# Optimization experiments

Hardware: AMD Instinct MI355X
Metric: run time of the kernel (lower is better)

The kernel has to match this reference:

```python
import jax, jax.numpy as jnp
import numpy as np

B, L, T = 512, 1024, 128  # batch, seq_len, n_tags


def setup_inputs() -> dict:
    key = jax.random.key(0)
    k1, k2, k3 = jax.random.split(key, 3)
    return {
        "emit_scores": jax.random.normal(k1, (B, L, T), dtype=jnp.float32),
        "transitions": jax.random.normal(k2, (T, T), dtype=jnp.float32),
        "tag_weight": jax.random.uniform(k3, (T,), dtype=jnp.float32),
    }


def _viterbi_single(emit, transitions):
    # emit: [L, T] (already scaled by tag_weight); transitions: [T, T]
    def step(prev, obs):
        # scores[i, j] = prev[i] + obs[j] + transitions[i, j]
        scores = prev[:, None] + obs[None, :] + transitions  # [T, T]
        return jnp.max(scores, axis=0), jnp.argmax(scores, axis=0).astype(jnp.int32)

    prev, bps = jax.lax.scan(step, emit[0], emit[1:])  # bps: [L-1, T]
    best_score = jnp.max(prev)
    last = jnp.argmax(prev).astype(jnp.int32)

    # Backtrace: path[t] = bps[t][path[t+1]], path[L-1] = last
    def back(idx, bp):
        nidx = bp[idx]
        return nidx, nidx

    _, rev_path = jax.lax.scan(back, last, bps, reverse=True)  # [L-1]
    path = jnp.concatenate([rev_path, last[None]])  # [L]
    return path, best_score


def reference(emit_scores, transitions, tag_weight):
    # emit_scores *= tag_weight (broadcast over tag dim), matching the torch code
    emit = emit_scores * tag_weight  # [B, L, T]
    path, best_score = jax.vmap(_viterbi_single, in_axes=(0, None))(emit, transitions)
    # path: [B, L] int32 tag indices (the original maps these to tag strings);
    # best_score: [B] Viterbi max score.
    return path, best_score
```

## Files before the change

kernel.cpp:

```cpp
#include <hip/hip_runtime.h>

#define B 512
#define L 1024
#define T 128
#define NROWS (L - 1)
#define SEG 64
#define NSEG 16

typedef unsigned char u8;
typedef float f2 __attribute__((ext_vector_type(2)));

#define M3(a, b, c) fmaxf(fmaxf((a), (b)), (c))

static __device__ __forceinline__ f2 pkadd(f2 a, f2 b) {
    f2 d;
    asm("v_pk_add_f32 %0, %1, %2" : "=v"(d) : "v"(a), "v"(b));
    return d;
}
static __device__ __forceinline__ float mx3(float a, float b, float c) {
    float d;
    asm("v_max3_f32 %0, %1, %2, %3" : "=v"(d) : "v"(a), "v"(b), "v"(c));
    return d;
}

#define DPPMAX(v, CTRL)                                                        \
    fmaxf((v), __int_as_float(__builtin_amdgcn_mov_dpp(                        \
                   __float_as_int(v), (CTRL), 0xf, 0xf, true)))
#define SWZMAX(v)                                                              \
    fmaxf((v), __int_as_float(__builtin_amdgcn_ds_swizzle(                     \
                   __float_as_int(v), 0x101F)))

#define BAR()                                                  \
    do {                                                       \
        asm volatile("s_waitcnt lgkmcnt(0)" ::: "memory");     \
        __builtin_amdgcn_s_barrier();                          \
        asm volatile("" ::: "memory");                         \
    } while (0)


__global__ __launch_bounds__(1024, 8) void viterbi_fwd_val(
    const float* __restrict__ emit, const float* __restrict__ trans,
    const float* __restrict__ w, float* __restrict__ out,
    float* __restrict__ prevws, int* __restrict__ lastTag)
{
    const int b   = blockIdx.x;
    const int tid = threadIdx.x;
    const int h   = tid & 7;
    const int j   = tid >> 3;
    const int hbase = h << 4;

    __shared__ __align__(16) float prevbuf[2 * T];
    __shared__ float swv[16];
    __shared__ int   swj[16];

    f2 tc2[8];
#pragma unroll
    for (int q = 0; q < 4; ++q) {
        f2 a, c;
        a.x = trans[(size_t)(hbase + 4 * q + 0) * T + j];
        a.y = trans[(size_t)(hbase + 4 * q + 1) * T + j];
        c.x = trans[(size_t)(hbase + 4 * q + 2) * T + j];
        c.y = trans[(size_t)(hbase + 4 * q + 3) * T + j];
        tc2[2 * q] = a; tc2[2 * q + 1] = c;
    }

    const float wj = w[j];
    const size_t ebase = (size_t)b * L * T;
    float* prow = prevws + (size_t)b * NROWS * T;

    const int ro0 = 16 * ((4 * h + 0) ^ ((h >> 1) & 3));
    const int ro1 = 16 * ((4 * h + 1) ^ ((h >> 1) & 3));
    const int ro2 = 16 * ((4 * h + 2) ^ ((h >> 1) & 3));
    const int ro3 = 16 * ((4 * h + 3) ^ ((h >> 1) & 3));
    const char* prdb = (const char*)prevbuf;
    char* pwr = (char*)prevbuf + 16 * ((j >> 2) ^ ((j >> 5) & 3)) + 4 * (j & 3);

    const float e0 = emit[ebase + j] * wj;
    if (h == 0) *(float*)pwr = e0;
    if (h == 1) prow[j] = e0;
    float myprev = e0;
    float r_c = emit[ebase + (size_t)T + j];
    float r_1 = emit[ebase + (size_t)2 * T + j];
    float bv_prev = 0.0f;
    BAR();

#define STEP(T_, ROFF_, WOFF_)                                                 \
    {                                                                          \
        const int t_ = (T_);                                                   \
        if (h == 1 && t_ >= 2)                        \
            prow[(size_t)(t_ - 1) * T + j] = bv_prev;                          \
        const int tn_ = (t_ + 2 < L) ? (t_ + 2) : (L - 1);                     \
        const float r_2 = emit[ebase + (size_t)tn_ * T + j];                   \
        const float obs_ = r_c * wj;                                           \
        f2 od_; od_.x = obs_; od_.y = obs_;                                    \
        const float4 p0 = *(const float4*)(prdb + (ROFF_) + ro0);              \
        const float4 p1 = *(const float4*)(prdb + (ROFF_) + ro1);              \
        const float4 p2 = *(const float4*)(prdb + (ROFF_) + ro2);              \
        const float4 p3 = *(const float4*)(prdb + (ROFF_) + ro3);              \
        f2 q0; q0.x = p0.x; q0.y = p0.y;                                       \
        f2 q1; q1.x = p0.z; q1.y = p0.w;                                       \
        f2 q2; q2.x = p1.x; q2.y = p1.y;                                       \
        f2 q3; q3.x = p1.z; q3.y = p1.w;                                       \
        f2 q4; q4.x = p2.x; q4.y = p2.y;                                       \
        f2 q5; q5.x = p2.z; q5.y = p2.w;                                       \
        f2 q6; q6.x = p3.x; q6.y = p3.y;                                       \
        f2 q7; q7.x = p3.z; q7.y = p3.w;                                       \
        const f2 v0 = pkadd(pkadd(q0, od_), tc2[0]);                           \
        const f2 v1 = pkadd(pkadd(q1, od_), tc2[1]);                           \
        const f2 v2 = pkadd(pkadd(q2, od_), tc2[2]);                           \
        const f2 v3 = pkadd(pkadd(q3, od_), tc2[3]);                           \
        const f2 v4 = pkadd(pkadd(q4, od_), tc2[4]);                           \
        const f2 v5 = pkadd(pkadd(q5, od_), tc2[5]);                           \
        const f2 v6 = pkadd(pkadd(q6, od_), tc2[6]);                           \
        const f2 v7 = pkadd(pkadd(q7, od_), tc2[7]);                           \
        const float m0 = mx3(v0.x, v0.y, v1.x);                               \
        const float m1 = mx3(v1.y, v2.x, v2.y);                               \
        const float m2 = mx3(v3.x, v3.y, v4.x);                               \
        const float m3 = mx3(v4.y, v5.x, v5.y);                               \
        const float m4 = mx3(v6.x, v6.y, v7.x);                               \
        const float n0 = mx3(m0, m1, m2);                                      \
        const float n1 = fmaxf(m3, m4);                                        \
        float bv = mx3(n0, n1, v7.y);                                          \
        bv = DPPMAX(bv, 0xB1);                          \
        bv = DPPMAX(bv, 0x4E);                          \
        bv = SWZMAX(bv);                               \
        if (h == 0) *(float*)(pwr + (WOFF_)) = bv;                             \
        myprev = bv;                                                           \
        bv_prev = bv;                                                          \
        r_c = r_1; r_1 = r_2;                                                  \
        BAR();                                                                 \
    }

    int t = 1;
    while (t + 1 < L) {
        STEP(t, 0, 512)
        STEP(t + 1, 512, 0)
        t += 2;
    }
    STEP(1023, 0, 512)
#undef STEP

    float rv = myprev; int rj = j;
#pragma unroll
    for (int m = 8; m <= 32; m <<= 1) {
        const float pv = __shfl_xor(rv, m);
        const int   pj = __shfl_xor(rj, m);
        if (pv > rv || (pv == rv && pj < rj)) { rv = pv; rj = pj; }
    }
    if ((tid & 63) == 0) { swv[tid >> 6] = rv; swj[tid >> 6] = rj; }
    __syncthreads();
    if (tid == 0) {
        float fv = swv[0]; int fj = swj[0];
#pragma unroll
        for (int wv = 1; wv < 16; ++wv) {
            if (swv[wv] > fv || (swv[wv] == fv && swj[wv] < fj)) {
                fv = swv[wv]; fj = swj[wv];
            }
        }
        out[(size_t)B * L + b] = fv;
        out[(size_t)b * L + (L - 1)] = (float)fj;
        lastTag[b] = fj;
    }
}

__global__ __launch_bounds__(64, 1) void backtrace(
    const float* __restrict__ emit, const float* __restrict__ trans,
    const float* __restrict__ w, const float* __restrict__ prevws,
    const int* __restrict__ lastTag, float* __restrict__ out)
{
    const int b = blockIdx.x;
    const int lane = threadIdx.x;
    __shared__ float transT[T * T];

#pragma unroll 4
    for (int it = 0; it < (T * T) / 64; ++it) {
        const int k = it * 64 + lane;
        const int i = k >> 7, jj = k & 127;
        transT[jj * T + (i ^ (jj & 31))] = trans[k];
    }

    const float w0 = w[lane], w1 = w[lane + 64];
    const size_t pbase = (size_t)b * NROWS * T;
    const size_t ebase = (size_t)b * L * T;
    const size_t obase = (size_t)b * L;

    float rp0[8], rp1[8], re0[8], re1[8];
#pragma unroll
    for (int k = 0; k < 8; ++k) {
        rp0[k] = prevws[pbase + (size_t)(1022 - k) * T + lane];
        rp1[k] = prevws[pbase + (size_t)(1022 - k) * T + lane + 64];
        re0[k] = emit[ebase + (size_t)(1023 - k) * T + lane];
        re1[k] = emit[ebase + (size_t)(1023 - k) * T + lane + 64];
    }

    int idx = lastTag[b];
    const float bsc = out[(size_t)B * L + b];
    float pp0 = bsc, pp1 = bsc;
    __syncthreads();

    int r = 1022;

#define BODY(U_)                                                               \
    {                                                                          \
        const float c0_ = rp0[U_], c1_ = rp1[U_];                              \
        const float e0_ = re0[U_], e1_ = re1[U_];                              \
        const int pr = (r >= 8) ? (r - 8) : 0;                                 \
        rp0[U_] = prevws[pbase + (size_t)pr * T + lane];                       \
        rp1[U_] = prevws[pbase + (size_t)pr * T + lane + 64];                  \
        re0[U_] = emit[ebase + (size_t)(pr + 1) * T + lane];                   \
        re1[U_] = emit[ebase + (size_t)(pr + 1) * T + lane + 64];              \
        const int sl = idx & 63;                                               \
        const bool lo = idx < 64;                                              \
        const float bv  = __shfl(lo ? pp0 : pp1, sl);                          \
        const float ew0 = e0_ * w0, ew1 = e1_ * w1;                            \
        const float obs = __shfl(lo ? ew0 : ew1, sl);                          \
        const int xc = lane ^ (idx & 31);                                      \
        const float t0 = transT[idx * T + xc];                                 \
        const float t1 = transT[idx * T + 64 + xc];                            \
        const float s0 = (c0_ + obs) + t0;                                     \
        const float s1 = (c1_ + obs) + t1;                                     \
        const unsigned long long m0 = __ballot(s0 == bv);                      \
        const unsigned long long m1 = __ballot(s1 == bv);                      \
        idx = (m0 != 0ULL) ? __builtin_ctzll(m0)                               \
                           : 64 + __builtin_ctzll(m1);                         \
        if (lane == 0) out[obase + r] = (float)idx;                            \
        pp0 = c0_; pp1 = c1_;                                                  \
        --r;                                                                   \
    }

#pragma unroll 1
    for (int g = 0; g < 127; ++g) {
        BODY(0) BODY(1) BODY(2) BODY(3) BODY(4) BODY(5) BODY(6) BODY(7)
    }
    BODY(0) BODY(1) BODY(2) BODY(3) BODY(4) BODY(5) BODY(6)
#undef BODY
}

__global__ __launch_bounds__(512, 4) void viterbi_fwd_slow(
    const float* __restrict__ emit, const float* __restrict__ trans,
    const float* __restrict__ w, float* __restrict__ out,
    u8* __restrict__ bps, int* __restrict__ lastTag)
{
    const int b   = blockIdx.x;
    const int tid = threadIdx.x;
    const int h   = tid & 3;
    const int j   = tid >> 2;
    const int hbase = h << 5;
    const bool lane0 = (h == 0);
    const int INF = 0x7fffffff;

    __shared__ __align__(16) float prevbuf[2 * T];
    __shared__ float swv[8];
    __shared__ int   swj[8];

    f2 tc2[16];
#pragma unroll
    for (int q = 0; q < 8; ++q) {
        f2 a, c;
        a.x = trans[(size_t)(hbase + 4 * q + 0) * T + j];
        a.y = trans[(size_t)(hbase + 4 * q + 1) * T + j];
        c.x = trans[(size_t)(hbase + 4 * q + 2) * T + j];
        c.y = trans[(size_t)(hbase + 4 * q + 3) * T + j];
        tc2[2 * q] = a; tc2[2 * q + 1] = c;
    }

    const float wj = w[j];
    const size_t ebase = (size_t)b * L * T;
    u8* bprow = bps + (size_t)b * NROWS * T;

    const char* prd = (const char*)prevbuf + 128 * h;
    char* pwr = (char*)prevbuf + 16 * ((j >> 2) ^ (j >> 5)) + 4 * (j & 3);

    const float e0 = emit[ebase + j] * wj;
    if (lane0) *(float*)pwr = e0;
    float myprev = e0;
    float raw_cur = emit[ebase + (size_t)T + j];
    int bidx_prev = 0;
    __syncthreads();

#define STEP(T_, ROFF_, WOFF_)                                                 \
    {                                                                          \
        const int t_ = (T_);                                                   \
        if (lane0 && t_ >= 2)                                                  \
            bprow[(size_t)(t_ - 2) * T + j] = (u8)bidx_prev;                   \
        const int tn_ = (t_ + 1 < L) ? (t_ + 1) : (L - 1);                     \
        const float raw_next_ = emit[ebase + (size_t)tn_ * T + j];             \
        const float obs_ = raw_cur * wj;                                       \
        f2 od_; od_.x = obs_; od_.y = obs_;                                    \
        f2 sv[16];                                                             \
        _Pragma("unroll")                                                      \
        for (int q = 0; q < 8; ++q) {                                          \
            const float4 p = *(const float4*)(prd + (ROFF_) + 16 * (q ^ h));   \
            f2 plo; plo.x = p.x; plo.y = p.y;                                  \
            f2 phi; phi.x = p.z; phi.y = p.w;                                  \
            sv[2 * q]     = (plo + od_) + tc2[2 * q];                          \
            sv[2 * q + 1] = (phi + od_) + tc2[2 * q + 1];                      \
        }                                                                      \
        float cm[4]; int loc[4];                                               \
        _Pragma("unroll")                                                      \
        for (int c = 0; c < 4; ++c) {                                          \
            const float s0 = sv[4 * c + 0].x, s1 = sv[4 * c + 0].y;            \
            const float s2 = sv[4 * c + 1].x, s3 = sv[4 * c + 1].y;            \
            const float s4 = sv[4 * c + 2].x, s5 = sv[4 * c + 2].y;            \
            const float s6 = sv[4 * c + 3].x, s7 = sv[4 * c + 3].y;            \
            const float m = M3(M3(s0, s1, s2), M3(s3, s4, s5),                 \
                               fmaxf(s6, s7));                                 \
            int k = 0;                                                         \
            k = (s7 == m) ? 7 : k; k = (s6 == m) ? 6 : k;                      \
            k = (s5 == m) ? 5 : k; k = (s4 == m) ? 4 : k;                      \
            k = (s3 == m) ? 3 : k; k = (s2 == m) ? 2 : k;                      \
            k = (s1 == m) ? 1 : k;                                             \
            cm[c] = m; loc[c] = 8 * c + k;                                     \
        }                                                                      \
        float bv = fmaxf(fmaxf(cm[0], cm[1]), fmaxf(cm[2], cm[3]));            \
        const int l0 = (cm[0] == bv) ? loc[0] : INF;                           \
        const int l1 = (cm[1] == bv) ? loc[1] : INF;                           \
        const int l2 = (cm[2] == bv) ? loc[2] : INF;                           \
        const int l3 = (cm[3] == bv) ? loc[3] : INF;                           \
        const int lm = min(min(min(l0, l1), l2), l3);                          \
        int gi = hbase + lm;                                                   \
        const float lv = bv;                                                   \
        bv = fmaxf(bv, __shfl_xor(bv, 1));                                     \
        bv = fmaxf(bv, __shfl_xor(bv, 2));                                     \
        int ii = (lv == bv) ? gi : INF;                                        \
        ii = min(ii, __shfl_xor(ii, 1));                                       \
        ii = min(ii, __shfl_xor(ii, 2));                                       \
        if (lane0) *(float*)(pwr + (WOFF_)) = bv;                              \
        myprev = bv;                                                           \
        bidx_prev = ii;                                                        \
        raw_cur = raw_next_;                                                   \
        __syncthreads();                                                       \
    }

    int t = 1;
    while (t + 1 < L) {
        STEP(t, 0, 512)
        STEP(t + 1, 512, 0)
        t += 2;
    }
    STEP(1023, 0, 512)
#undef STEP

    if (lane0) bprow[(size_t)(NROWS - 1) * T + j] = (u8)bidx_prev;

    float rv = myprev; int rj = j;
#pragma unroll
    for (int m = 4; m <= 32; m <<= 1) {
        const float pv = __shfl_xor(rv, m);
        const int   pj = __shfl_xor(rj, m);
        if (pv > rv || (pv == rv && pj < rj)) { rv = pv; rj = pj; }
    }
    if ((tid & 63) == 0) { swv[tid >> 6] = rv; swj[tid >> 6] = rj; }
    __syncthreads();
    if (tid == 0) {
        float fv = swv[0]; int fj = swj[0];
#pragma unroll
        for (int wv = 1; wv < 8; ++wv) {
            if (swv[wv] > fv || (swv[wv] == fv && swj[wv] < fj)) {
                fv = swv[wv]; fj = swj[wv];
            }
        }
        out[(size_t)B * L + b] = fv;
        out[(size_t)b * L + (L - 1)] = (float)fj;
        lastTag[b] = fj;
    }
}

__global__ __launch_bounds__(T) void segcomp(const u8* __restrict__ bps,
                                             u8* __restrict__ comp)
{
    const int s = blockIdx.x & (NSEG - 1);
    const int b = blockIdx.x >> 4;
    const int r0 = s * SEG;
    const int cnt = (NROWS - r0 < SEG) ? (NROWS - r0) : SEG;

    __shared__ __align__(16) u8 rows[SEG * T];
    const uint4* src = (const uint4*)(bps + ((size_t)b * NROWS + r0) * T);
    uint4* dst = (uint4*)rows;
    const int nvec = cnt * (T / 16);
    for (int k = threadIdx.x; k < nvec; k += T) dst[k] = src[k];
    __syncthreads();

    int x = threadIdx.x;
    for (int k = cnt - 1; k >= 0; --k) x = rows[k * T + x];
    comp[((size_t)b * NSEG + s) * T + threadIdx.x] = (u8)x;
}

__global__ void chainseg(const u8* __restrict__ comp,
                         const int* __restrict__ lastTag,
                         float* __restrict__ out)
{
    const int b = blockIdx.x * blockDim.x + threadIdx.x;
    if (b >= B) return;
    int e = lastTag[b];
#pragma unroll 1
    for (int s = NSEG - 1; s >= 0; --s) {
        e = comp[((size_t)b * NSEG + s) * T + e];
        out[(size_t)b * L + s * SEG] = (float)e;
    }
}

__global__ __launch_bounds__(T) void fillseg(const u8* __restrict__ bps,
                                             const int* __restrict__ lastTag,
                                             float* __restrict__ out)
{
    const int s = blockIdx.x & (NSEG - 1);
    const int b = blockIdx.x >> 4;
    const int r0 = s * SEG;
    const int cnt = (NROWS - r0 < SEG) ? (NROWS - r0) : SEG;

    __shared__ __align__(16) u8 rows[SEG * T];
    const uint4* src = (const uint4*)(bps + ((size_t)b * NROWS + r0) * T);
    uint4* dst = (uint4*)rows;
    const int nvec = cnt * (T / 16);
    for (int k = threadIdx.x; k < nvec; k += T) dst[k] = src[k];
    __syncthreads();

    if (threadIdx.x == 0) {
        int e = (s == NSEG - 1) ? lastTag[b]
                                : (int)out[(size_t)b * L + (size_t)(s + 1) * SEG];
        for (int k = cnt - 1; k >= 1; --k) {
            e = rows[k * T + e];
            out[(size_t)b * L + r0 + k] = (float)e;
        }
    }
}

extern "C" void kernel_launch(void* const* d_in, const int* in_sizes, int n_in,
                              void* d_out, int out_size, void* d_ws, size_t ws_size,
                              hipStream_t stream)
{
    const float* emit  = (const float*)d_in[0];
    const float* trans = (const float*)d_in[1];
    const float* w     = (const float*)d_in[2];
    float* out = (float*)d_out;

    const size_t prev_bytes = (size_t)B * NROWS * T * sizeof(float);
    const size_t need_fast  = prev_bytes + B * sizeof(int);

    if (ws_size >= need_fast) {
        float* prevws  = (float*)d_ws;
        int*   lastTag = (int*)((char*)d_ws + prev_bytes);
        viterbi_fwd_val<<<B, 1024, 0, stream>>>(emit, trans, w, out, prevws, lastTag);
        backtrace<<<B, 64, 0, stream>>>(emit, trans, w, prevws, lastTag, out);
    } else {
        u8*  bps     = (u8*)d_ws;
        u8*  comp    = bps + (size_t)B * NROWS * T;
        int* lastTag = (int*)(comp + (size_t)B * NSEG * T);
        viterbi_fwd_slow<<<B, 512, 0, stream>>>(emit, trans, w, out, bps, lastTag);
        segcomp<<<B * NSEG, T, 0, stream>>>(bps, comp);
        chainseg<<<2, 256, 0, stream>>>(comp, lastTag, out);
        fillseg<<<B * NSEG, T, 0, stream>>>(bps, lastTag, out);
    }
}
```

Baseline: 882.6 us.

## Process two batch sequences per block to interleave independent Viterbi chains

The forward Viterbi kernel now handles two batch elements per 1024-thread block. It keeps two shared prev buffers and computes both candidate maxima between the same barriers. This halves the grid and amortises each barrier and its latency over two independent recurrences, giving more instruction-level parallelism per step. In exchange each step does twice the work, register pressure rises (launch bounds lowered to 4), and the final reduction is run twice with extra syncs.

```diff
diff --git a/kernel.cpp b/kernel.cpp
--- a/kernel.cpp
+++ b/kernel.cpp
@@ -38,18 +38,20 @@
     } while (0)
 
 
-__global__ __launch_bounds__(1024, 8) void viterbi_fwd_val(
+__global__ __launch_bounds__(1024, 4) void viterbi_fwd_val(
     const float* __restrict__ emit, const float* __restrict__ trans,
     const float* __restrict__ w, float* __restrict__ out,
     float* __restrict__ prevws, int* __restrict__ lastTag)
 {
-    const int b   = blockIdx.x;
     const int tid = threadIdx.x;
     const int h   = tid & 7;
     const int j   = tid >> 3;
     const int hbase = h << 4;
-
-    __shared__ __align__(16) float prevbuf[2 * T];
+    const int bA  = 2 * blockIdx.x;
+    const int bB  = bA + 1;
+
+    __shared__ __align__(16) float bufA[2 * T];
+    __shared__ __align__(16) float bufB[2 * T];
     __shared__ float swv[16];
     __shared__ int   swj[16];
 
@@ -65,38 +67,41 @@
     }
 
     const float wj = w[j];
-    const size_t ebase = (size_t)b * L * T;
-    float* prow = prevws + (size_t)b * NROWS * T;
+    const size_t ebA = (size_t)bA * L * T;
+    const size_t ebB = (size_t)bB * L * T;
+    float* prA = prevws + (size_t)bA * NROWS * T;
+    float* prB = prevws + (size_t)bB * NROWS * T;
 
     const int ro0 = 16 * ((4 * h + 0) ^ ((h >> 1) & 3));
     const int ro1 = 16 * ((4 * h + 1) ^ ((h >> 1) & 3));
     const int ro2 = 16 * ((4 * h + 2) ^ ((h >> 1) & 3));
     const int ro3 = 16 * ((4 * h + 3) ^ ((h >> 1) & 3));
-    const char* prdb = (const char*)prevbuf;
-    char* pwr = (char*)prevbuf + 16 * ((j >> 2) ^ ((j >> 5) & 3)) + 4 * (j & 3);
-
-    const float e0 = emit[ebase + j] * wj;
-    if (h == 0) *(float*)pwr = e0;
-    if (h == 1) prow[j] = e0;
-    float myprev = e0;
-    float r_c = emit[ebase + (size_t)T + j];
-    float r_1 = emit[ebase + (size_t)2 * T + j];
-    float bv_prev = 0.0f;
+    const char* pbA = (const char*)bufA;
+    const char* pbB = (const char*)bufB;
+    const int wo = 16 * ((j >> 2) ^ ((j >> 5) & 3)) + 4 * (j & 3);
+    char* pwA = (char*)bufA + wo;
+    char* pwB = (char*)bufB + wo;
+
+    const float e0A = emit[ebA + j] * wj;
+    const float e0B = emit[ebB + j] * wj;
+    if (h == 0) { *(float*)pwA = e0A; *(float*)pwB = e0B; }
+    if (h == 1) prA[j] = e0A;
+    if (h == 2) prB[j] = e0B;
+    float mA = e0A, mB = e0B;
+    float rcA = emit[ebA + (size_t)T + j];
+    float r1A = emit[ebA + (size_t)2 * T + j];
+    float rcB = emit[ebB + (size_t)T + j];
+    float r1B = emit[ebB + (size_t)2 * T + j];
+    float bpA = 0.0f, bpB = 0.0f;
     BAR();
 
-#define STEP(T_, ROFF_, WOFF_)                                                 \
+#define CAND(PB_, ROFF_, BV_)                                                  \
+    float BV_;                                                                 \
     {                                                                          \
-        const int t_ = (T_);                                                   \
-        if (h == 1 && t_ >= 2)                        \
-            prow[(size_t)(t_ - 1) * T + j] = bv_prev;                          \
-        const int tn_ = (t_ + 2 < L) ? (t_ + 2) : (L - 1);                     \
-        const float r_2 = emit[ebase + (size_t)tn_ * T + j];                   \
-        const float obs_ = r_c * wj;                                           \
-        f2 od_; od_.x = obs_; od_.y = obs_;                                    \
-        const float4 p0 = *(const float4*)(prdb + (ROFF_) + ro0);              \
-        const float4 p1 = *(const float4*)(prdb + (ROFF_) + ro1);              \
-        const float4 p2 = *(const float4*)(prdb + (ROFF_) + ro2);              \
-        const float4 p3 = *(const float4*)(prdb + (ROFF_) + ro3);              \
+        const float4 p0 = *(const float4*)((PB_) + (ROFF_) + ro0);             \
+        const float4 p1 = *(const float4*)((PB_) + (ROFF_) + ro1);             \
+        const float4 p2 = *(const float4*)((PB_) + (ROFF_) + ro2);             \
+        const float4 p3 = *(const float4*)((PB_) + (ROFF_) + ro3);             \
         f2 q0; q0.x = p0.x; q0.y = p0.y;                                       \
         f2 q1; q1.x = p0.z; q1.y = p0.w;                                       \
         f2 q2; q2.x = p1.x; q2.y = p1.y;                                       \
@@ -105,29 +110,53 @@
         f2 q5; q5.x = p2.z; q5.y = p2.w;                                       \
         f2 q6; q6.x = p3.x; q6.y = p3.y;                                       \
         f2 q7; q7.x = p3.z; q7.y = p3.w;                                       \
-        const f2 v0 = pkadd(pkadd(q0, od_), tc2[0]);                           \
-        const f2 v1 = pkadd(pkadd(q1, od_), tc2[1]);                           \
-        const f2 v2 = pkadd(pkadd(q2, od_), tc2[2]);                           \
-        const f2 v3 = pkadd(pkadd(q3, od_), tc2[3]);                           \
-        const f2 v4 = pkadd(pkadd(q4, od_), tc2[4]);                           \
-        const f2 v5 = pkadd(pkadd(q5, od_), tc2[5]);                           \
-        const f2 v6 = pkadd(pkadd(q6, od_), tc2[6]);                           \
-        const f2 v7 = pkadd(pkadd(q7, od_), tc2[7]);                           \
-        const float m0 = mx3(v0.x, v0.y, v1.x);                               \
-        const float m1 = mx3(v1.y, v2.x, v2.y);                               \
-        const float m2 = mx3(v3.x, v3.y, v4.x);                               \
-        const float m3 = mx3(v4.y, v5.x, v5.y);                               \
-        const float m4 = mx3(v6.x, v6.y, v7.x);                               \
+        const f2 v0 = pkadd(pkadd(q0, od), tc2[0]);                            \
+        const f2 v1 = pkadd(pkadd(q1, od), tc2[1]);                            \
+        const f2 v2 = pkadd(pkadd(q2, od), tc2[2]);                            \
+        const f2 v3 = pkadd(pkadd(q3, od), tc2[3]);                            \
+        const f2 v4 = pkadd(pkadd(q4, od), tc2[4]);                            \
+        const f2 v5 = pkadd(pkadd(q5, od), tc2[5]);                            \
+        const f2 v6 = pkadd(pkadd(q6, od), tc2[6]);                            \
+        const f2 v7 = pkadd(pkadd(q7, od), tc2[7]);                            \
+        const float m0 = mx3(v0.x, v0.y, v1.x);                                \
+        const float m1 = mx3(v1.y, v2.x, v2.y);                                \
+        const float m2 = mx3(v3.x, v3.y, v4.x);                                \
+        const float m3 = mx3(v4.y, v5.x, v5.y);                                \
+        const float m4 = mx3(v6.x, v6.y, v7.x);                                \
         const float n0 = mx3(m0, m1, m2);                                      \
         const float n1 = fmaxf(m3, m4);                                        \
-        float bv = mx3(n0, n1, v7.y);                                          \
-        bv = DPPMAX(bv, 0xB1);                          \
-        bv = DPPMAX(bv, 0x4E);                          \
-        bv = SWZMAX(bv);                               \
-        if (h == 0) *(float*)(pwr + (WOFF_)) = bv;                             \
-        myprev = bv;                                                           \
-        bv_prev = bv;                                                          \
-        r_c = r_1; r_1 = r_2;                                                  \
+        BV_ = mx3(n0, n1, v7.y);                                               \
+    }
+
+#define STEP(T_, ROFF_, WOFF_)                                                 \
+    {                                                                          \
+        const int t_ = (T_);                                                   \
+        if (h == 1 && t_ >= 2) prA[(size_t)(t_ - 1) * T + j] = bpA;            \
+        if (h == 2 && t_ >= 2) prB[(size_t)(t_ - 1) * T + j] = bpB;            \
+        const int tn_ = (t_ + 2 < L) ? (t_ + 2) : (L - 1);                     \
+        const float r2A = emit[ebA + (size_t)tn_ * T + j];                     \
+        const float r2B = emit[ebB + (size_t)tn_ * T + j];                     \
+        {                                                                      \
+            const float obsA = rcA * wj;                                       \
+            f2 od; od.x = obsA; od.y = obsA;                                   \
+            CAND(pbA, ROFF_, bvA0)                                             \
+            float bvA = bvA0;                                                  \
+            const float obsB = rcB * wj;                                       \
+            od.x = obsB; od.y = obsB;                                          \
+            CAND(pbB, ROFF_, bvB0)                                             \
+            float bvB = bvB0;                                                  \
+            bvA = DPPMAX(bvA, 0xB1); bvB = DPPMAX(bvB, 0xB1);                  \
+            bvA = DPPMAX(bvA, 0x4E); bvB = DPPMAX(bvB, 0x4E);                  \
+            bvA = SWZMAX(bvA);       bvB = SWZMAX(bvB);                        \
+            if (h == 0) {                                                      \
+                *(float*)(pwA + (WOFF_)) = bvA;                                \
+                *(float*)(pwB + (WOFF_)) = bvB;                                \
+            }                                                                  \
+            mA = bvA; mB = bvB;                                                \
+            bpA = bvA; bpB = bvB;                                              \
+        }                                                                      \
+        rcA = r1A; r1A = r2A;                                                  \
+        rcB = r1B; r1B = r2B;                                                  \
         BAR();                                                                 \
     }
 
@@ -139,28 +168,36 @@
     }
     STEP(1023, 0, 512)
 #undef STEP
-
-    float rv = myprev; int rj = j;
-#pragma unroll
-    for (int m = 8; m <= 32; m <<= 1) {
-        const float pv = __shfl_xor(rv, m);
-        const int   pj = __shfl_xor(rj, m);
-        if (pv > rv || (pv == rv && pj < rj)) { rv = pv; rj = pj; }
-    }
-    if ((tid & 63) == 0) { swv[tid >> 6] = rv; swj[tid >> 6] = rj; }
-    __syncthreads();
-    if (tid == 0) {
-        float fv = swv[0]; int fj = swj[0];
-#pragma unroll
-        for (int wv = 1; wv < 16; ++wv) {
-            if (swv[wv] > fv || (swv[wv] == fv && swj[wv] < fj)) {
-                fv = swv[wv]; fj = swj[wv];
-            }
-        }
-        out[(size_t)B * L + b] = fv;
-        out[(size_t)b * L + (L - 1)] = (float)fj;
-        lastTag[b] = fj;
-    }
+#undef CAND
+
+#define FINRED(MV_, BX_)                                                       \
+    {                                                                          \
+        float rv = (MV_); int rj = j;                                          \
+        _Pragma("unroll")                                                      \
+        for (int m = 8; m <= 32; m <<= 1) {                                    \
+            const float pv = __shfl_xor(rv, m);                                \
+            const int   pj = __shfl_xor(rj, m);                                \
+            if (pv > rv || (pv == rv && pj < rj)) { rv = pv; rj = pj; }        \
+        }                                                                      \
+        if ((tid & 63) == 0) { swv[tid >> 6] = rv; swj[tid >> 6] = rj; }       \
+        __syncthreads();                                                       \
+        if (tid == 0) {                                                        \
+            float fv = swv[0]; int fj = swj[0];                                \
+            _Pragma("unroll")                                                  \
+            for (int wv = 1; wv < 16; ++wv) {                                  \
+                if (swv[wv] > fv || (swv[wv] == fv && swj[wv] < fj)) {         \
+                    fv = swv[wv]; fj = swj[wv];                                \
+                }                                                              \
+            }                                                                  \
+            out[(size_t)B * L + (BX_)] = fv;                                   \
+            out[(size_t)(BX_) * L + (L - 1)] = (float)fj;                      \
+            lastTag[(BX_)] = fj;                                               \
+        }                                                                      \
+        __syncthreads();                                                       \
+    }
+    FINRED(mA, bA)
+    FINRED(mB, bB)
+#undef FINRED
 }
 
 __global__ __launch_bounds__(64, 1) void backtrace(
@@ -441,7 +478,7 @@
     if (ws_size >= need_fast) {
         float* prevws  = (float*)d_ws;
         int*   lastTag = (int*)((char*)d_ws + prev_bytes);
-        viterbi_fwd_val<<<B, 1024, 0, stream>>>(emit, trans, w, out, prevws, lastTag);
+        viterbi_fwd_val<<<B / 2, 1024, 0, stream>>>(emit, trans, w, out, prevws, lastTag);
         backtrace<<<B, 64, 0, stream>>>(emit, trans, w, prevws, lastTag, out);
     } else {
         u8*  bps     = (u8*)d_ws;
```

Result: slower. 974.4 us (+10.4%).
